# Performance work log

Measured on AMD Instinct MI355X. Metric: run time of the kernel, lower is better.

Reference implementation:

```python
import jax, jax.numpy as jnp
import numpy as np

NUM_HEADS = 16

def phi(x):
    return jax.nn.elu(x) + 1.0

def setup_inputs() -> dict:
    key = jax.random.key(0)
    ks = jax.random.split(key, 8)
    B, Tq, Tk, H = 4, 8192, 8192, 1024
    s = 1.0 / np.sqrt(H)
    return {
        "q": jax.random.normal(ks[0], (B, Tq, H), jnp.float32),
        "k": jax.random.normal(ks[1], (B, Tk, H), jnp.float32),
        "v": jax.random.normal(ks[2], (B, Tk, H), jnp.float32),
        "mask": jnp.ones((B, Tk), jnp.float32),
        "Wq": jax.random.normal(ks[3], (H, H), jnp.float32) * s,
        "Wk": jax.random.normal(ks[4], (H, H), jnp.float32) * s,
        "Wv": jax.random.normal(ks[5], (H, H), jnp.float32) * s,
        "Wo": jax.random.normal(ks[6], (H, H), jnp.float32) * s,
    }

def reference(q, k, v, mask, Wq, Wk, Wv, Wo):
    B, Tq, H = q.shape
    Tk = k.shape[1]
    nh = NUM_HEADS
    d = H // nh
    # projections (torch Linear: x @ W.T), split heads -> bhtd
    Q = (q @ Wq.T).reshape(B, Tq, nh, d).transpose(0, 2, 1, 3)
    K = (k @ Wk.T).reshape(B, Tk, nh, d).transpose(0, 2, 1, 3)
    V = (v @ Wv.T).reshape(B, Tk, nh, d).transpose(0, 2, 1, 3)
    Q = phi(Q)
    K = phi(K)
    m = mask[:, None, :, None]  # b1t1
    K = K * m
    V = V * m
    K_sum = K.sum(axis=2)                          # bhd
    KV = jnp.einsum('bhtd,bhtv->bhdv', K, V)       # bh d d
    Z = 1.0 / (jnp.einsum('bhtd,bhd->bht', Q, K_sum) + 1e-6)
    out = jnp.einsum('bhtd,bhdv->bhtv', Q, KV) * Z[..., None]
    out = out.transpose(0, 2, 1, 3).reshape(B, Tq, H)
    return out @ Wo.T
```

## Files before the change

### kernel.cpp

```cpp
#include <hip/hip_runtime.h>
#include <hip/hip_bf16.h>
#include <stdint.h>

#define B_  4
#define T_  8192
#define H_  1024
#define NH_ 16
#define D_  64
#define BT_ (B_*T_)

typedef __attribute__((ext_vector_type(8))) __bf16 bf16x8;
typedef __attribute__((ext_vector_type(4))) __bf16 bf16x4;
typedef __attribute__((ext_vector_type(4))) float  f32x4;

__device__ __forceinline__ float phi_f(float x) {
    return x > 0.0f ? x + 1.0f : __expf(x);
}

__device__ __forceinline__ void async_copy16(const void* g, void* l) {
    __builtin_amdgcn_global_load_lds(
        (const __attribute__((address_space(1))) uint32_t*)g,
        (__attribute__((address_space(3))) uint32_t*)l, 16, 0, 0);
}

__global__ void conv_bf16(const float* __restrict__ src, __bf16* __restrict__ dst) {
    size_t i = ((size_t)blockIdx.x * 256 + threadIdx.x) * 8;
    float4 a = *(const float4*)(src + i);
    float4 b = *(const float4*)(src + i + 4);
    bf16x8 o;
    o[0]=(__bf16)a.x; o[1]=(__bf16)a.y; o[2]=(__bf16)a.z; o[3]=(__bf16)a.w;
    o[4]=(__bf16)b.x; o[5]=(__bf16)b.y; o[6]=(__bf16)b.z; o[7]=(__bf16)b.w;
    *(bf16x8*)(dst + i) = o;
}

__global__ void wconv4(const float* __restrict__ s0, const float* __restrict__ s1,
                       const float* __restrict__ s2, const float* __restrict__ s3,
                       __bf16* __restrict__ d0, __bf16* __restrict__ d1,
                       __bf16* __restrict__ d2, __bf16* __restrict__ d3) {
    const float* s; __bf16* d;
    switch (blockIdx.y) {
        case 0: s = s0; d = d0; break;
        case 1: s = s1; d = d1; break;
        case 2: s = s2; d = d2; break;
        default: s = s3; d = d3; break;
    }
    int i = (blockIdx.x * 256 + threadIdx.x) * 4;
    float4 v = *(const float4*)(s + i);
    bf16x4 o;
    o[0] = (__bf16)v.x; o[1] = (__bf16)v.y; o[2] = (__bf16)v.z; o[3] = (__bf16)v.w;
    *(bf16x4*)(d + i) = o;
}

template<int EPI>
__global__ __launch_bounds__(256, 2)
void gemm_bt(const __bf16* __restrict__ A, const __bf16* __restrict__ Wb,
             const float* __restrict__ mask, const float* __restrict__ aux,
             void* __restrict__ OutV)
{
    const int orig = blockIdx.x;
    const int wgid = (orig & 7) * 256 + (orig >> 3);
    const int bm = (wgid >> 3) * 128;
    const int bn = (wgid & 7) * 128;
    const int tid  = threadIdx.x;
    const int lane = tid & 63;
    const int wid  = tid >> 6;
    const int wm = wid >> 1, wn = wid & 1;

    const __bf16* Wp = Wb;
    if (EPI == 3) Wp = Wb + ((size_t)(bm >> 13) << 20);

    __shared__ __bf16 Al[128 * 64];
    __shared__ __bf16 Bl[128 * 64];

    f32x4 acc[4][4];
    #pragma unroll
    for (int i = 0; i < 4; ++i)
        #pragma unroll
        for (int j = 0; j < 4; ++j) acc[i][j] = (f32x4)0.0f;

    const int sn = wid * 8 + (lane >> 3);
    const int sc = (lane & 7) * 16;

    for (int k0 = 0; k0 < H_; k0 += 64) {
        #pragma unroll
        for (int issue = 0; issue < 4; ++issue) {
            int n = issue * 32 + sn;
            int csw = sc ^ ((n & 7) << 4);
            async_copy16((const char*)(A  + (size_t)(bm + n) * H_ + k0) + csw,
                         (char*)Al + issue * 4096 + wid * 1024);
            async_copy16((const char*)(Wp + (size_t)(bn + n) * H_ + k0) + csw,
                         (char*)Bl + issue * 4096 + wid * 1024);
        }
        __syncthreads();
        #pragma unroll
        for (int ks = 0; ks < 2; ++ks) {
            bf16x8 afr[4], bfr[4];
            #pragma unroll
            for (int mi = 0; mi < 4; ++mi) {
                int r  = wm * 64 + mi * 16 + (lane & 15);
                int cb = (ks * 64 + (lane >> 4) * 16) ^ ((r & 7) << 4);
                afr[mi] = *(const bf16x8*)((const char*)Al + r * 128 + cb);
            }
            #pragma unroll
            for (int ni = 0; ni < 4; ++ni) {
                int r  = wn * 64 + ni * 16 + (lane & 15);
                int cb = (ks * 64 + (lane >> 4) * 16) ^ ((r & 7) << 4);
                bfr[ni] = *(const bf16x8*)((const char*)Bl + r * 128 + cb);
            }
            #pragma unroll
            for (int mi = 0; mi < 4; ++mi)
                #pragma unroll
                for (int ni = 0; ni < 4; ++ni)
                    acc[mi][ni] = __builtin_amdgcn_mfma_f32_16x16x32_bf16(
                        afr[mi], bfr[ni], acc[mi][ni], 0, 0, 0);
        }
        __syncthreads();
    }
    const int gm0 = bm + wm * 64;
    const int gn0 = bn + wn * 64 + (lane & 15);

    if (EPI == 0) {
        const int b = bm >> 13;
        const int h = (bn >> 6) + wn;
        float ksv[4];
        #pragma unroll
        for (int ni = 0; ni < 4; ++ni)
            ksv[ni] = aux[((b * 16 + h) << 6) + ni * 16 + (lane & 15)];
        #pragma unroll
        for (int mi = 0; mi < 4; ++mi) {
            #pragma unroll
            for (int j = 0; j < 4; ++j) {
                float pv[4], s = 0.0f;
                #pragma unroll
                for (int ni = 0; ni < 4; ++ni) {
                    pv[ni] = phi_f(acc[mi][ni][j]);
                    s += pv[ni] * ksv[ni];
                }
                s += __shfl_xor(s, 1);
                s += __shfl_xor(s, 2);
                s += __shfl_xor(s, 4);
                s += __shfl_xor(s, 8);
                float z = 1.0f / (s + 1e-6f);
                int gm = gm0 + mi * 16 + (lane >> 4) * 4 + j;
                __bf16* op = (__bf16*)OutV + (size_t)gm * H_ + gn0;
                #pragma unroll
                for (int ni = 0; ni < 4; ++ni)
                    op[ni * 16] = (__bf16)(pv[ni] * z);
            }
        }
    } else {
        #pragma unroll
        for (int mi = 0; mi < 4; ++mi) {
            #pragma unroll
            for (int j = 0; j < 4; ++j) {
                int gm = gm0 + mi * 16 + (lane >> 4) * 4 + j;
                if (EPI == 3) {
                    float* op = (float*)OutV + (size_t)gm * H_ + gn0;
                    #pragma unroll
                    for (int ni = 0; ni < 4; ++ni)
                        op[ni * 16] = acc[mi][ni][j];
                } else {
                    float mv = mask[gm];
                    __bf16* op = (__bf16*)OutV + (size_t)gm * H_ + gn0;
                    #pragma unroll
                    for (int ni = 0; ni < 4; ++ni) {
                        float v = acc[mi][ni][j];
                        if (EPI == 1) v = phi_f(v) * mv;
                        else          v = v * mv;
                        op[ni * 16] = (__bf16)v;
                    }
                }
            }
        }
    }
}

__global__ __launch_bounds__(256, 2)
void kv_kernel(const __bf16* __restrict__ Kb, const __bf16* __restrict__ Vb,
               float* __restrict__ KVp, float* __restrict__ Ksp)
{
    const int chunk = blockIdx.x;
    const int bh = blockIdx.y;
    const int b = bh >> 4, h = bh & 15;
    const int tid = threadIdx.x, lane = tid & 63, wid = tid >> 6;

    __shared__ char KtRaw[64 * 144];
    __shared__ char VtRaw[64 * 144];
    __shared__ float ksbuf[32][64];

    const int st  = tid >> 3;
    const int dkg = tid & 7;
    const int dk0 = dkg * 8;
    const int swzT = (dkg & 7) << 4;

    f32x4 acc[4];
    #pragma unroll
    for (int i = 0; i < 4; ++i) acc[i] = (f32x4)0.0f;
    float ksacc[8];
    #pragma unroll
    for (int i = 0; i < 8; ++i) ksacc[i] = 0.0f;

    const size_t gbase = ((size_t)b * T_ + (size_t)chunk * 1024) * H_
                         + h * 64 + dk0;

    bf16x8 ka, kc, va, vc;
    {
        const __bf16* p  = Kb + gbase;
        const __bf16* pv = Vb + gbase;
        ka = *(const bf16x8*)(p  + (size_t)st * H_);
        kc = *(const bf16x8*)(p  + (size_t)(st + 32) * H_);
        va = *(const bf16x8*)(pv + (size_t)st * H_);
        vc = *(const bf16x8*)(pv + (size_t)(st + 32) * H_);
    }

    for (int tile = 0; tile < 16; ++tile) {
        __syncthreads();
        #pragma unroll
        for (int j = 0; j < 8; ++j) {
            int rowb = (dk0 + j) * 144;
            *(__bf16*)(KtRaw + ((rowb + 2*st)        ^ swzT)) = ka[j];
            *(__bf16*)(KtRaw + ((rowb + 2*(st + 32)) ^ swzT)) = kc[j];
            *(__bf16*)(VtRaw + ((rowb + 2*st)        ^ swzT)) = va[j];
            *(__bf16*)(VtRaw + ((rowb + 2*(st + 32)) ^ swzT)) = vc[j];
            ksacc[j] += (float)ka[j] + (float)kc[j];
        }
        if (tile < 15) {
            const __bf16* p  = Kb + gbase + (size_t)(tile + 1) * 64 * H_;
            const __bf16* pv = Vb + gbase + (size_t)(tile + 1) * 64 * H_;
            ka = *(const bf16x8*)(p  + (size_t)st * H_);
            kc = *(const bf16x8*)(p  + (size_t)(st + 32) * H_);
            va = *(const bf16x8*)(pv + (size_t)st * H_);
            vc = *(const bf16x8*)(pv + (size_t)(st + 32) * H_);
        }
        __syncthreads();
        #pragma unroll
        for (int ks = 0; ks < 2; ++ks) {
            int r = wid * 16 + (lane & 15);
            int cb = (r * 144 + (ks * 64 + (lane >> 4) * 16)) ^ (((r >> 3) & 7) << 4);
            bf16x8 af = *(const bf16x8*)(KtRaw + cb);
            #pragma unroll
            for (int ni = 0; ni < 4; ++ni) {
                int rv = ni * 16 + (lane & 15);
                int cv = (rv * 144 + (ks * 64 + (lane >> 4) * 16)) ^ (((rv >> 3) & 7) << 4);
                bf16x8 bf = *(const bf16x8*)(VtRaw + cv);
                acc[ni] = __builtin_amdgcn_mfma_f32_16x16x32_bf16(af, bf, acc[ni], 0, 0, 0);
            }
        }
    }

    float* kvp = KVp + ((size_t)chunk * 64 + bh) * 4096;
    #pragma unroll
    for (int ni = 0; ni < 4; ++ni)
        #pragma unroll
        for (int jj = 0; jj < 4; ++jj) {
            int dk = wid * 16 + (lane >> 4) * 4 + jj;
            int dv = ni * 16 + (lane & 15);
            kvp[dk * 64 + dv] = acc[ni][jj];
        }

    #pragma unroll
    for (int j = 0; j < 8; ++j)
        ksbuf[st][dk0 + j] = ksacc[j];
    __syncthreads();
    if (tid < 64) {
        float s = 0.0f;
        #pragma unroll 8
        for (int st2 = 0; st2 < 32; ++st2) s += ksbuf[st2][tid];
        Ksp[((size_t)chunk * 64 + bh) * 64 + tid] = s;
    }
}

__global__ void kvsum(const float* __restrict__ KVp, const float* __restrict__ Ksp,
                      __bf16* __restrict__ KVb, float* __restrict__ Ks) {
    int bh = blockIdx.x, tid = threadIdx.x;
    __bf16* d = KVb + (size_t)bh * 4096;
    for (int i = tid; i < 4096; i += 256) {
        float s = 0.0f;
        #pragma unroll
        for (int c = 0; c < 8; ++c)
            s += KVp[((size_t)c * 64 + bh) * 4096 + i];
        d[i] = (__bf16)s;
    }
    if (tid < 64) {
        float s = 0.0f;
        #pragma unroll
        for (int c = 0; c < 8; ++c)
            s += Ksp[((size_t)c * 64 + bh) * 64 + tid];
        Ks[bh * 64 + tid] = s;
    }
}

__global__ __launch_bounds__(256)
void ugemm(const __bf16* __restrict__ Wob, const __bf16* __restrict__ KVb,
           __bf16* __restrict__ Ut)
{
    const int mp = blockIdx.x, bhp = blockIdx.y;
    const int b = bhp >> 3, hp = bhp & 7;
    const int tid = threadIdx.x, lane = tid & 63, w = tid >> 6;
    const int wm = w >> 1, wn = w & 1;
    const int h = hp * 2 + wn;
    const int bm = mp * 128;
    const int lane15 = lane & 15;

    __shared__ __bf16 As[128][136];
    __shared__ __bf16 Bs[2][64][72];

    {
        int r = tid >> 1, c0 = (tid & 1) * 64;
        const __bf16* src = Wob + (size_t)(bm + r) * H_ + hp * 128 + c0;
        #pragma unroll
        for (int j = 0; j < 8; ++j)
            *(bf16x8*)&As[r][c0 + j*8] = *(const bf16x8*)(src + j*8);
    }
    {
        int hh = tid >> 7, idx = tid & 127, r = idx >> 1, c0 = (idx & 1) * 32;
        const __bf16* src = KVb + ((size_t)(b * 16 + hp * 2 + hh) * 64 + r) * 64 + c0;
        #pragma unroll
        for (int j = 0; j < 4; ++j)
            *(bf16x8*)&Bs[hh][r][c0 + j*8] = *(const bf16x8*)(src + j*8);
    }
    __syncthreads();

    f32x4 acc[4][4];
    #pragma unroll
    for (int i = 0; i < 4; ++i)
        #pragma unroll
        for (int j = 0; j < 4; ++j) acc[i][j] = (f32x4)0.0f;

    #pragma unroll
    for (int ks = 0; ks < 2; ++ks) {
        bf16x8 afr[4], bfr[4];
        #pragma unroll
        for (int mi = 0; mi < 4; ++mi)
            afr[mi] = *(const bf16x8*)&As[wm*64 + mi*16 + lane15]
                                         [wn*64 + ks*32 + (lane>>4)*8];
        #pragma unroll
        for (int ni = 0; ni < 4; ++ni)
            bfr[ni] = *(const bf16x8*)&Bs[wn][ni*16 + lane15]
                                         [ks*32 + (lane>>4)*8];
        #pragma unroll
        for (int mi = 0; mi < 4; ++mi)
            #pragma unroll
            for (int ni = 0; ni < 4; ++ni)
                acc[mi][ni] = __builtin_amdgcn_mfma_f32_16x16x32_bf16(
                    afr[mi], bfr[ni], acc[mi][ni], 0, 0, 0);
    }

    __bf16* up = Ut + ((size_t)b << 20);
    #pragma unroll
    for (int mi = 0; mi < 4; ++mi)
        #pragma unroll
        for (int j = 0; j < 4; ++j) {
            int m2 = bm + wm * 64 + mi * 16 + (lane >> 4) * 4 + j;
            #pragma unroll
            for (int ni = 0; ni < 4; ++ni) {
                int dk = ni * 16 + lane15;
                up[(size_t)m2 * H_ + h * 64 + dk] = (__bf16)acc[mi][ni][j];
            }
        }
}

extern "C" void kernel_launch(void* const* d_in, const int* in_sizes, int n_in,
                              void* d_out, int out_size, void* d_ws, size_t ws_size,
                              hipStream_t stream) {
    (void)in_sizes; (void)n_in; (void)out_size; (void)ws_size;
    const float* q    = (const float*)d_in[0];
    const float* k    = (const float*)d_in[1];
    const float* v    = (const float*)d_in[2];
    const float* mask = (const float*)d_in[3];
    const float* Wq   = (const float*)d_in[4];
    const float* Wk   = (const float*)d_in[5];
    const float* Wv   = (const float*)d_in[6];
    const float* Wo   = (const float*)d_in[7];
    float* out = (float*)d_out;

    char* ws = (char*)d_ws;
    const size_t WELEM = (size_t)H_ * H_;
    const size_t PELEM = (size_t)BT_ * H_;
    __bf16* Wqb = (__bf16*)ws;
    __bf16* Wkb = Wqb + WELEM;
    __bf16* Wvb = Wkb + WELEM;
    __bf16* Wob = Wvb + WELEM;
    __bf16* Qb  = Wob + WELEM;
    __bf16* Kb  = Qb + PELEM;
    __bf16* Vb  = Kb + PELEM;
    __bf16* tmp = Vb + PELEM;
    float*  KVp = (float*)(tmp + PELEM);
    float*  Ksp = KVp + (size_t)8 * 64 * 4096;
    float*  Ksf = Ksp + (size_t)8 * 64 * 64;
    __bf16* KVb = (__bf16*)(Ksf + (size_t)64 * 64);
    __bf16* Ut  = (__bf16*)KVp;

    wconv4<<<dim3(1024, 4), 256, 0, stream>>>(Wq, Wk, Wv, Wo, Wqb, Wkb, Wvb, Wob);

    const int cgrid = (int)(PELEM / (256 * 8));
    conv_bf16<<<cgrid, 256, 0, stream>>>(k, tmp);
    gemm_bt<1><<<2048, 256, 0, stream>>>(tmp, Wkb, mask, nullptr, Kb);
    conv_bf16<<<cgrid, 256, 0, stream>>>(v, tmp);
    gemm_bt<2><<<2048, 256, 0, stream>>>(tmp, Wvb, mask, nullptr, Vb);

    kv_kernel<<<dim3(T_/1024, B_*NH_), 256, 0, stream>>>(Kb, Vb, KVp, Ksp);
    kvsum<<<B_*NH_, 256, 0, stream>>>(KVp, Ksp, KVb, Ksf);
    ugemm<<<dim3(8, 32), 256, 0, stream>>>(Wob, KVb, Ut);

    conv_bf16<<<cgrid, 256, 0, stream>>>(q, tmp);
    gemm_bt<0><<<2048, 256, 0, stream>>>(tmp, Wqb, mask, Ksf, Qb);
    gemm_bt<3><<<2048, 256, 0, stream>>>(Qb, (const __bf16*)Ut, mask, nullptr, out);
}
```

Before: 431.7 us.

## Fuse fp32-to-bf16 activation conversion into projection GEMM A-tile loads

New measurement: 630.2 us. +46.0%, slower.

```diff
diff --git a/kernel.cpp b/kernel.cpp
--- a/kernel.cpp
+++ b/kernel.cpp
@@ -21,16 +21,6 @@
     __builtin_amdgcn_global_load_lds(
         (const __attribute__((address_space(1))) uint32_t*)g,
         (__attribute__((address_space(3))) uint32_t*)l, 16, 0, 0);
-}
-
-__global__ void conv_bf16(const float* __restrict__ src, __bf16* __restrict__ dst) {
-    size_t i = ((size_t)blockIdx.x * 256 + threadIdx.x) * 8;
-    float4 a = *(const float4*)(src + i);
-    float4 b = *(const float4*)(src + i + 4);
-    bf16x8 o;
-    o[0]=(__bf16)a.x; o[1]=(__bf16)a.y; o[2]=(__bf16)a.z; o[3]=(__bf16)a.w;
-    o[4]=(__bf16)b.x; o[5]=(__bf16)b.y; o[6]=(__bf16)b.z; o[7]=(__bf16)b.w;
-    *(bf16x8*)(dst + i) = o;
 }
 
 __global__ void wconv4(const float* __restrict__ s0, const float* __restrict__ s1,
@@ -53,9 +43,9 @@
 
 template<int EPI>
 __global__ __launch_bounds__(256, 2)
-void gemm_bt(const __bf16* __restrict__ A, const __bf16* __restrict__ Wb,
-             const float* __restrict__ mask, const float* __restrict__ aux,
-             void* __restrict__ OutV)
+void gemm_f32a(const float* __restrict__ A, const __bf16* __restrict__ Wb,
+               const float* __restrict__ mask, const float* __restrict__ aux,
+               __bf16* __restrict__ Out)
 {
     const int orig = blockIdx.x;
     const int wgid = (orig & 7) * 256 + (orig >> 3);
@@ -66,10 +56,7 @@
     const int wid  = tid >> 6;
     const int wm = wid >> 1, wn = wid & 1;
 
-    const __bf16* Wp = Wb;
-    if (EPI == 3) Wp = Wb + ((size_t)(bm >> 13) << 20);
-
-    __shared__ __bf16 Al[128 * 64];
+    __shared__ __bf16 Al[128 * 72];
     __shared__ __bf16 Bl[128 * 64];
 
     f32x4 acc[4][4];
@@ -77,6 +64,11 @@
     for (int i = 0; i < 4; ++i)
         #pragma unroll
         for (int j = 0; j < 4; ++j) acc[i][j] = (f32x4)0.0f;
+
+    const int ar = tid >> 1;
+    const int ah = (tid & 1) * 32;
+    const float* aptr = A + (size_t)(bm + ar) * H_ + ah;
+    char* alw = (char*)Al + ar * 144 + ah * 2;
 
     const int sn = wid * 8 + (lane >> 3);
     const int sc = (lane & 7) * 16;
@@ -86,10 +78,22 @@
         for (int issue = 0; issue < 4; ++issue) {
             int n = issue * 32 + sn;
             int csw = sc ^ ((n & 7) << 4);
-            async_copy16((const char*)(A  + (size_t)(bm + n) * H_ + k0) + csw,
-                         (char*)Al + issue * 4096 + wid * 1024);
-            async_copy16((const char*)(Wp + (size_t)(bn + n) * H_ + k0) + csw,
+            async_copy16((const char*)(Wb + (size_t)(bn + n) * H_ + k0) + csw,
                          (char*)Bl + issue * 4096 + wid * 1024);
+        }
+        {
+            const float* ap = aptr + k0;
+            float4 av[8];
+            #pragma unroll
+            for (int i = 0; i < 8; ++i) av[i] = ((const float4*)ap)[i];
+            #pragma unroll
+            for (int j = 0; j < 4; ++j) {
+                float4 x = av[2*j], y = av[2*j+1];
+                bf16x8 t;
+                t[0]=(__bf16)x.x; t[1]=(__bf16)x.y; t[2]=(__bf16)x.z; t[3]=(__bf16)x.w;
+                t[4]=(__bf16)y.x; t[5]=(__bf16)y.y; t[6]=(__bf16)y.z; t[7]=(__bf16)y.w;
+                *(bf16x8*)(alw + j * 16) = t;
+            }
         }
         __syncthreads();
         #pragma unroll
@@ -97,9 +101,8 @@
             bf16x8 afr[4], bfr[4];
             #pragma unroll
             for (int mi = 0; mi < 4; ++mi) {
-                int r  = wm * 64 + mi * 16 + (lane & 15);
-                int cb = (ks * 64 + (lane >> 4) * 16) ^ ((r & 7) << 4);
-                afr[mi] = *(const bf16x8*)((const char*)Al + r * 128 + cb);
+                int r = wm * 64 + mi * 16 + (lane & 15);
+                afr[mi] = *(const bf16x8*)((const char*)Al + r * 144 + ks * 64 + (lane >> 4) * 16);
             }
             #pragma unroll
             for (int ni = 0; ni < 4; ++ni) {
@@ -142,7 +145,7 @@
                 s += __shfl_xor(s, 8);
                 float z = 1.0f / (s + 1e-6f);
                 int gm = gm0 + mi * 16 + (lane >> 4) * 4 + j;
-                __bf16* op = (__bf16*)OutV + (size_t)gm * H_ + gn0;
+                __bf16* op = Out + (size_t)gm * H_ + gn0;
                 #pragma unroll
                 for (int ni = 0; ni < 4; ++ni)
                     op[ni * 16] = (__bf16)(pv[ni] * z);
@@ -154,25 +157,94 @@
             #pragma unroll
             for (int j = 0; j < 4; ++j) {
                 int gm = gm0 + mi * 16 + (lane >> 4) * 4 + j;
-                if (EPI == 3) {
-                    float* op = (float*)OutV + (size_t)gm * H_ + gn0;
-                    #pragma unroll
-                    for (int ni = 0; ni < 4; ++ni)
-                        op[ni * 16] = acc[mi][ni][j];
-                } else {
-                    float mv = mask[gm];
-                    __bf16* op = (__bf16*)OutV + (size_t)gm * H_ + gn0;
-                    #pragma unroll
-                    for (int ni = 0; ni < 4; ++ni) {
-                        float v = acc[mi][ni][j];
-                        if (EPI == 1) v = phi_f(v) * mv;
-                        else          v = v * mv;
-                        op[ni * 16] = (__bf16)v;
-                    }
+                float mv = mask[gm];
+                __bf16* op = Out + (size_t)gm * H_ + gn0;
+                #pragma unroll
+                for (int ni = 0; ni < 4; ++ni) {
+                    float v = acc[mi][ni][j];
+                    if (EPI == 1) v = phi_f(v) * mv;
+                    else          v = v * mv;
+                    op[ni * 16] = (__bf16)v;
                 }
             }
         }
     }
+}
+
+__global__ __launch_bounds__(256, 2)
+void gemm_fin(const __bf16* __restrict__ A, const __bf16* __restrict__ Wb,
+              float* __restrict__ Out)
+{
+    const int orig = blockIdx.x;
+    const int wgid = (orig & 7) * 256 + (orig >> 3);
+    const int bm = (wgid >> 3) * 128;
+    const int bn = (wgid & 7) * 128;
+    const int tid  = threadIdx.x;
+    const int lane = tid & 63;
+    const int wid  = tid >> 6;
+    const int wm = wid >> 1, wn = wid & 1;
+
+    const __bf16* Wp = Wb + ((size_t)(bm >> 13) << 20);
+
+    __shared__ __bf16 Al[128 * 64];
+    __shared__ __bf16 Bl[128 * 64];
+
+    f32x4 acc[4][4];
+    #pragma unroll
+    for (int i = 0; i < 4; ++i)
+        #pragma unroll
+        for (int j = 0; j < 4; ++j) acc[i][j] = (f32x4)0.0f;
+
+    const int sn = wid * 8 + (lane >> 3);
+    const int sc = (lane & 7) * 16;
+
+    for (int k0 = 0; k0 < H_; k0 += 64) {
+        #pragma unroll
+        for (int issue = 0; issue < 4; ++issue) {
+            int n = issue * 32 + sn;
+            int csw = sc ^ ((n & 7) << 4);
+            async_copy16((const char*)(A  + (size_t)(bm + n) * H_ + k0) + csw,
+                         (char*)Al + issue * 4096 + wid * 1024);
+            async_copy16((const char*)(Wp + (size_t)(bn + n) * H_ + k0) + csw,
+                         (char*)Bl + issue * 4096 + wid * 1024);
+        }
+        __syncthreads();
+        #pragma unroll
+        for (int ks = 0; ks < 2; ++ks) {
+            bf16x8 afr[4], bfr[4];
+            #pragma unroll
+            for (int mi = 0; mi < 4; ++mi) {
+                int r  = wm * 64 + mi * 16 + (lane & 15);
+                int cb = (ks * 64 + (lane >> 4) * 16) ^ ((r & 7) << 4);
+                afr[mi] = *(const bf16x8*)((const char*)Al + r * 128 + cb);
+            }
+            #pragma unroll
+            for (int ni = 0; ni < 4; ++ni) {
+                int r  = wn * 64 + ni * 16 + (lane & 15);
+                int cb = (ks * 64 + (lane >> 4) * 16) ^ ((r & 7) << 4);
+                bfr[ni] = *(const bf16x8*)((const char*)Bl + r * 128 + cb);
+            }
+            #pragma unroll
+            for (int mi = 0; mi < 4; ++mi)
+                #pragma unroll
+                for (int ni = 0; ni < 4; ++ni)
+                    acc[mi][ni] = __builtin_amdgcn_mfma_f32_16x16x32_bf16(
+                        afr[mi], bfr[ni], acc[mi][ni], 0, 0, 0);
+        }
+        __syncthreads();
+    }
+    const int gm0 = bm + wm * 64;
+    const int gn0 = bn + wn * 64 + (lane & 15);
+    #pragma unroll
+    for (int mi = 0; mi < 4; ++mi)
+        #pragma unroll
+        for (int j = 0; j < 4; ++j) {
+            int gm = gm0 + mi * 16 + (lane >> 4) * 4 + j;
+            float* op = Out + (size_t)gm * H_ + gn0;
+            #pragma unroll
+            for (int ni = 0; ni < 4; ++ni)
+                op[ni * 16] = acc[mi][ni][j];
+        }
 }
 
 __global__ __launch_bounds__(256, 2)
@@ -384,8 +456,7 @@
     __bf16* Qb  = Wob + WELEM;
     __bf16* Kb  = Qb + PELEM;
     __bf16* Vb  = Kb + PELEM;
-    __bf16* tmp = Vb + PELEM;
-    float*  KVp = (float*)(tmp + PELEM);
+    float*  KVp = (float*)(Vb + PELEM);
     float*  Ksp = KVp + (size_t)8 * 64 * 4096;
     float*  Ksf = Ksp + (size_t)8 * 64 * 64;
     __bf16* KVb = (__bf16*)(Ksf + (size_t)64 * 64);
@@ -393,17 +464,13 @@
 
     wconv4<<<dim3(1024, 4), 256, 0, stream>>>(Wq, Wk, Wv, Wo, Wqb, Wkb, Wvb, Wob);
 
-    const int cgrid = (int)(PELEM / (256 * 8));
-    conv_bf16<<<cgrid, 256, 0, stream>>>(k, tmp);
-    gemm_bt<1><<<2048, 256, 0, stream>>>(tmp, Wkb, mask, nullptr, Kb);
-    conv_bf16<<<cgrid, 256, 0, stream>>>(v, tmp);
-    gemm_bt<2><<<2048, 256, 0, stream>>>(tmp, Wvb, mask, nullptr, Vb);
+    gemm_f32a<1><<<2048, 256, 0, stream>>>(k, Wkb, mask, nullptr, Kb);
+    gemm_f32a<2><<<2048, 256, 0, stream>>>(v, Wvb, mask, nullptr, Vb);
 
     kv_kernel<<<dim3(T_/1024, B_*NH_), 256, 0, stream>>>(Kb, Vb, KVp, Ksp);
     kvsum<<<B_*NH_, 256, 0, stream>>>(KVp, Ksp, KVb, Ksf);
     ugemm<<<dim3(8, 32), 256, 0, stream>>>(Wob, KVb, Ut);
 
-    conv_bf16<<<cgrid, 256, 0, stream>>>(q, tmp);
-    gemm_bt<0><<<2048, 256, 0, stream>>>(tmp, Wqb, mask, Ksf, Qb);
-    gemm_bt<3><<<2048, 256, 0, stream>>>(Qb, (const __bf16*)Ut, mask, nullptr, out);
-}
+    gemm_f32a<0><<<2048, 256, 0, stream>>>(q, Wqb, mask, Ksf, Qb);
+    gemm_fin<<<2048, 256, 0, stream>>>(Qb, Ut, out);
+}
```

## Overlap next input fp32-to-bf16 conversion with projection GEMMs via extra blocks

Applied to the files above, without the earlier changes.

Result: slower. 459.8 us (+6.5%).

```diff
diff --git a/kernel.cpp b/kernel.cpp
--- a/kernel.cpp
+++ b/kernel.cpp
@@ -51,12 +51,24 @@
     *(bf16x4*)(d + i) = o;
 }
 
-template<int EPI>
+template<int EPI, int NCONV>
 __global__ __launch_bounds__(256, 2)
 void gemm_bt(const __bf16* __restrict__ A, const __bf16* __restrict__ Wb,
              const float* __restrict__ mask, const float* __restrict__ aux,
-             void* __restrict__ OutV)
+             void* __restrict__ OutV,
+             const float* __restrict__ csrc, __bf16* __restrict__ cdst)
 {
+    if (NCONV && blockIdx.x >= 2048) {
+        size_t i = ((size_t)(blockIdx.x - 2048) * 256 + threadIdx.x) * 8;
+        float4 a = *(const float4*)(csrc + i);
+        float4 b = *(const float4*)(csrc + i + 4);
+        bf16x8 o;
+        o[0]=(__bf16)a.x; o[1]=(__bf16)a.y; o[2]=(__bf16)a.z; o[3]=(__bf16)a.w;
+        o[4]=(__bf16)b.x; o[5]=(__bf16)b.y; o[6]=(__bf16)b.z; o[7]=(__bf16)b.w;
+        *(bf16x8*)(cdst + i) = o;
+        return;
+    }
+
     const int orig = blockIdx.x;
     const int wgid = (orig & 7) * 256 + (orig >> 3);
     const int bm = (wgid >> 3) * 128;
@@ -381,11 +393,12 @@
     __bf16* Wkb = Wqb + WELEM;
     __bf16* Wvb = Wkb + WELEM;
     __bf16* Wob = Wvb + WELEM;
-    __bf16* Qb  = Wob + WELEM;
-    __bf16* Kb  = Qb + PELEM;
-    __bf16* Vb  = Kb + PELEM;
-    __bf16* tmp = Vb + PELEM;
-    float*  KVp = (float*)(tmp + PELEM);
+    __bf16* Kb   = Wob + WELEM;
+    __bf16* Vb   = Kb + PELEM;
+    __bf16* tmp1 = Vb + PELEM;
+    __bf16* tmp2 = tmp1 + PELEM;
+    __bf16* Qb   = tmp2;
+    float*  KVp = (float*)(tmp2 + PELEM);
     float*  Ksp = KVp + (size_t)8 * 64 * 4096;
     float*  Ksf = Ksp + (size_t)8 * 64 * 64;
     __bf16* KVb = (__bf16*)(Ksf + (size_t)64 * 64);
@@ -394,16 +407,15 @@
     wconv4<<<dim3(1024, 4), 256, 0, stream>>>(Wq, Wk, Wv, Wo, Wqb, Wkb, Wvb, Wob);
 
     const int cgrid = (int)(PELEM / (256 * 8));
-    conv_bf16<<<cgrid, 256, 0, stream>>>(k, tmp);
-    gemm_bt<1><<<2048, 256, 0, stream>>>(tmp, Wkb, mask, nullptr, Kb);
-    conv_bf16<<<cgrid, 256, 0, stream>>>(v, tmp);
-    gemm_bt<2><<<2048, 256, 0, stream>>>(tmp, Wvb, mask, nullptr, Vb);
+    conv_bf16<<<cgrid, 256, 0, stream>>>(k, tmp1);
+
+    gemm_bt<1, 1><<<2048 + 16384, 256, 0, stream>>>(tmp1, Wkb, mask, nullptr, Kb, v, tmp2);
+    gemm_bt<2, 1><<<2048 + 16384, 256, 0, stream>>>(tmp2, Wvb, mask, nullptr, Vb, q, tmp1);
 
     kv_kernel<<<dim3(T_/1024, B_*NH_), 256, 0, stream>>>(Kb, Vb, KVp, Ksp);
     kvsum<<<B_*NH_, 256, 0, stream>>>(KVp, Ksp, KVb, Ksf);
     ugemm<<<dim3(8, 32), 256, 0, stream>>>(Wob, KVb, Ut);
 
-    conv_bf16<<<cgrid, 256, 0, stream>>>(q, tmp);
-    gemm_bt<0><<<2048, 256, 0, stream>>>(tmp, Wqb, mask, Ksf, Qb);
-    gemm_bt<3><<<2048, 256, 0, stream>>>(Qb, (const __bf16*)Ut, mask, nullptr, out);
-}
+    gemm_bt<0, 0><<<2048, 256, 0, stream>>>(tmp1, Wqb, mask, Ksf, Qb, nullptr, nullptr);
+    gemm_bt<3, 0><<<2048, 256, 0, stream>>>(Qb, Ut, mask, nullptr, out, nullptr, nullptr);
+}
```

## Replace final output GEMM with 256x256-tile double-buffered pipelined kernel

Applied to the files above, without the earlier changes.

New measurement: 468.9 us. +8.6%, slower.

```diff
diff --git a/kernel.cpp b/kernel.cpp
--- a/kernel.cpp
+++ b/kernel.cpp
@@ -12,6 +12,8 @@
 typedef __attribute__((ext_vector_type(8))) __bf16 bf16x8;
 typedef __attribute__((ext_vector_type(4))) __bf16 bf16x4;
 typedef __attribute__((ext_vector_type(4))) float  f32x4;
+
+template<int N> struct IC { static constexpr int v = N; };
 
 __device__ __forceinline__ float phi_f(float x) {
     return x > 0.0f ? x + 1.0f : __expf(x);
@@ -55,7 +57,7 @@
 __global__ __launch_bounds__(256, 2)
 void gemm_bt(const __bf16* __restrict__ A, const __bf16* __restrict__ Wb,
              const float* __restrict__ mask, const float* __restrict__ aux,
-             void* __restrict__ OutV)
+             __bf16* __restrict__ Out)
 {
     const int orig = blockIdx.x;
     const int wgid = (orig & 7) * 256 + (orig >> 3);
@@ -66,9 +68,6 @@
     const int wid  = tid >> 6;
     const int wm = wid >> 1, wn = wid & 1;
 
-    const __bf16* Wp = Wb;
-    if (EPI == 3) Wp = Wb + ((size_t)(bm >> 13) << 20);
-
     __shared__ __bf16 Al[128 * 64];
     __shared__ __bf16 Bl[128 * 64];
 
@@ -88,7 +87,7 @@
             int csw = sc ^ ((n & 7) << 4);
             async_copy16((const char*)(A  + (size_t)(bm + n) * H_ + k0) + csw,
                          (char*)Al + issue * 4096 + wid * 1024);
-            async_copy16((const char*)(Wp + (size_t)(bn + n) * H_ + k0) + csw,
+            async_copy16((const char*)(Wb + (size_t)(bn + n) * H_ + k0) + csw,
                          (char*)Bl + issue * 4096 + wid * 1024);
         }
         __syncthreads();
@@ -142,7 +141,7 @@
                 s += __shfl_xor(s, 8);
                 float z = 1.0f / (s + 1e-6f);
                 int gm = gm0 + mi * 16 + (lane >> 4) * 4 + j;
-                __bf16* op = (__bf16*)OutV + (size_t)gm * H_ + gn0;
+                __bf16* op = Out + (size_t)gm * H_ + gn0;
                 #pragma unroll
                 for (int ni = 0; ni < 4; ++ni)
                     op[ni * 16] = (__bf16)(pv[ni] * z);
@@ -154,25 +153,150 @@
             #pragma unroll
             for (int j = 0; j < 4; ++j) {
                 int gm = gm0 + mi * 16 + (lane >> 4) * 4 + j;
-                if (EPI == 3) {
-                    float* op = (float*)OutV + (size_t)gm * H_ + gn0;
-                    #pragma unroll
-                    for (int ni = 0; ni < 4; ++ni)
-                        op[ni * 16] = acc[mi][ni][j];
-                } else {
-                    float mv = mask[gm];
-                    __bf16* op = (__bf16*)OutV + (size_t)gm * H_ + gn0;
-                    #pragma unroll
-                    for (int ni = 0; ni < 4; ++ni) {
-                        float v = acc[mi][ni][j];
-                        if (EPI == 1) v = phi_f(v) * mv;
-                        else          v = v * mv;
-                        op[ni * 16] = (__bf16)v;
-                    }
+                float mv = mask[gm];
+                __bf16* op = Out + (size_t)gm * H_ + gn0;
+                #pragma unroll
+                for (int ni = 0; ni < 4; ++ni) {
+                    float v = acc[mi][ni][j];
+                    if (EPI == 1) v = phi_f(v) * mv;
+                    else          v = v * mv;
+                    op[ni * 16] = (__bf16)v;
                 }
             }
         }
     }
+}
+
+__global__ __launch_bounds__(512, 2)
+void gemm256_fin(const __bf16* __restrict__ A, const __bf16* __restrict__ Wb,
+                 float* __restrict__ Out)
+{
+    __shared__ __align__(16) char lds[131072];
+
+    const int orig = blockIdx.x;
+    const int wg = (orig & 7) * 64 + (orig >> 3);
+    const int bm = (wg >> 2) * 256;
+    const int bn = (wg & 3) * 256;
+    const int tid = threadIdx.x, lane = tid & 63, w = tid >> 6;
+    const int wm = w >> 2, wn = w & 3;
+    const int lane15 = lane & 15, q = lane >> 4;
+
+    const __bf16* Wp = Wb + ((size_t)(bm >> 13) << 20);
+
+    const int srow = tid & 255;
+    const char* gA0 = (const char*)(A  + (size_t)(bm + srow) * H_) + (tid >> 8) * 16;
+    const char* gB0 = (const char*)(Wp + (size_t)(bn + srow) * H_) + (tid >> 8) * 16;
+    const int d0 = w * 1024;
+
+    auto ST = [&](int buf, int isB, int hk, int kt) {
+        const int kb = kt * 128 + hk * 64;
+        const char* s = isB ? gB0 : gA0;
+        char* d = (char*)lds + buf * 65536 + isB * 32768 + hk * 16384 + d0;
+        async_copy16(s + kb, d);
+        async_copy16(s + kb + 32, d + 8192);
+    };
+
+    f32x4 acc[8][4];
+    #pragma unroll
+    for (int i = 0; i < 8; ++i)
+        #pragma unroll
+        for (int j = 0; j < 4; ++j) acc[i][j] = (f32x4)0.0f;
+
+    const int arowoff = (wm * 128 + lane15) * 16;
+    const int browoff = (wn * 64  + lane15) * 16;
+
+    bf16x8 aF[8], bF[4];
+
+    auto body = [&](auto dbc, int kt, int sn1, int sn2, int wmode) {
+        constexpr int DB = decltype(dbc)::v;
+        const char* base = (const char*)lds + DB * 65536 + q * 4096;
+        #pragma unroll
+        for (int mi = 0; mi < 8; ++mi)
+            aF[mi] = *(const bf16x8*)(base + arowoff + mi * 256);
+        #pragma unroll
+        for (int ni = 0; ni < 4; ++ni)
+            bF[ni] = *(const bf16x8*)(base + 32768 + browoff + ni * 256);
+        if (sn1) ST(DB ^ 1, 1, 1, kt + 1);
+        __builtin_amdgcn_s_barrier();
+        __builtin_amdgcn_s_setprio(1);
+        #pragma unroll
+        for (int mi = 0; mi < 4; ++mi)
+            #pragma unroll
+            for (int ni = 0; ni < 4; ++ni)
+                acc[mi][ni] = __builtin_amdgcn_mfma_f32_16x16x32_bf16(
+                    aF[mi], bF[ni], acc[mi][ni], 0, 0, 0);
+        __builtin_amdgcn_s_setprio(0);
+        __builtin_amdgcn_s_barrier();
+        if (sn2) ST(DB, 0, 0, kt + 2);
+        __builtin_amdgcn_s_barrier();
+        __builtin_amdgcn_s_setprio(1);
+        #pragma unroll
+        for (int mi = 4; mi < 8; ++mi)
+            #pragma unroll
+            for (int ni = 0; ni < 4; ++ni)
+                acc[mi][ni] = __builtin_amdgcn_mfma_f32_16x16x32_bf16(
+                    aF[mi], bF[ni], acc[mi][ni], 0, 0, 0);
+        __builtin_amdgcn_s_setprio(0);
+        __builtin_amdgcn_s_barrier();
+        #pragma unroll
+        for (int mi = 0; mi < 8; ++mi)
+            aF[mi] = *(const bf16x8*)(base + 16384 + arowoff + mi * 256);
+        #pragma unroll
+        for (int ni = 0; ni < 4; ++ni)
+            bF[ni] = *(const bf16x8*)(base + 49152 + browoff + ni * 256);
+        if (sn2) ST(DB, 1, 0, kt + 2);
+        __builtin_amdgcn_s_barrier();
+        __builtin_amdgcn_s_setprio(1);
+        #pragma unroll
+        for (int mi = 0; mi < 4; ++mi)
+            #pragma unroll
+            for (int ni = 0; ni < 4; ++ni)
+                acc[mi][ni] = __builtin_amdgcn_mfma_f32_16x16x32_bf16(
+                    aF[mi], bF[ni], acc[mi][ni], 0, 0, 0);
+        __builtin_amdgcn_s_setprio(0);
+        __builtin_amdgcn_s_barrier();
+        if (sn2) ST(DB, 0, 1, kt + 2);
+        if (wmode == 0)      asm volatile("s_waitcnt vmcnt(6)" ::: "memory");
+        else if (wmode == 1) asm volatile("s_waitcnt vmcnt(0)" ::: "memory");
+        __builtin_amdgcn_s_barrier();
+        __builtin_amdgcn_s_setprio(1);
+        #pragma unroll
+        for (int mi = 4; mi < 8; ++mi)
+            #pragma unroll
+            for (int ni = 0; ni < 4; ++ni)
+                acc[mi][ni] = __builtin_amdgcn_mfma_f32_16x16x32_bf16(
+                    aF[mi], bF[ni], acc[mi][ni], 0, 0, 0);
+        __builtin_amdgcn_s_setprio(0);
+        __builtin_amdgcn_s_barrier();
+    };
+
+    ST(0, 0, 0, 0); ST(0, 1, 0, 0); ST(0, 0, 1, 0); ST(0, 1, 1, 0);
+    ST(1, 0, 0, 1); ST(1, 1, 0, 1); ST(1, 0, 1, 1);
+    asm volatile("s_waitcnt vmcnt(6)" ::: "memory");
+    __builtin_amdgcn_s_barrier();
+
+    #pragma unroll 1
+    for (int kt2 = 0; kt2 < 12; kt2 += 2) {
+        body(IC<0>{}, kt2,     1, 1, 0);
+        body(IC<1>{}, kt2 + 1, 1, 1, 0);
+    }
+    body(IC<0>{}, 12, 1, 1, 0);
+    body(IC<1>{}, 13, 1, 1, 0);
+    body(IC<0>{}, 14, 1, 0, 1);
+    body(IC<1>{}, 15, 0, 0, 2);
+
+    const int gm0 = bm + wm * 128;
+    const int gn0 = bn + wn * 64 + lane15;
+    #pragma unroll
+    for (int mi = 0; mi < 8; ++mi)
+        #pragma unroll
+        for (int j = 0; j < 4; ++j) {
+            int gm = gm0 + mi * 16 + (lane >> 4) * 4 + j;
+            float* op = Out + (size_t)gm * H_ + gn0;
+            #pragma unroll
+            for (int ni = 0; ni < 4; ++ni)
+                op[ni * 16] = acc[mi][ni][j];
+        }
 }
 
 __global__ __launch_bounds__(256, 2)
@@ -405,5 +529,6 @@
 
     conv_bf16<<<cgrid, 256, 0, stream>>>(q, tmp);
     gemm_bt<0><<<2048, 256, 0, stream>>>(tmp, Wqb, mask, Ksf, Qb);
-    gemm_bt<3><<<2048, 256, 0, stream>>>(Qb, (const __bf16*)Ut, mask, nullptr, out);
-}
+
+    gemm256_fin<<<512, 512, 0, stream>>>(Qb, Ut, out);
+}
```
